# Kernel optimization log

Measured on AMD Instinct MI355X. Metric: run time of the kernel, lower is better.

The kernel has to match this reference:

```python
import jax, jax.numpy as jnp
import numpy as np

D_IN = 1024
D_OUT = 1024

def setup_inputs() -> dict:
    key = jax.random.key(0)
    ks = jax.random.split(key, 7)
    s = 1.0 / np.sqrt(D_IN)
    x = jax.random.normal(ks[0], (4, 2048, D_IN), dtype=jnp.float32)
    Wq = jax.random.uniform(ks[1], (D_IN, D_OUT), jnp.float32, -s, s)
    bq = jax.random.uniform(ks[2], (D_OUT,), jnp.float32, -s, s)
    Wk = jax.random.uniform(ks[3], (D_IN, D_OUT), jnp.float32, -s, s)
    bk = jax.random.uniform(ks[4], (D_OUT,), jnp.float32, -s, s)
    Wv = jax.random.uniform(ks[5], (D_IN, D_OUT), jnp.float32, -s, s)
    bv = jax.random.uniform(ks[6], (D_OUT,), jnp.float32, -s, s)
    return {"x": x, "Wq": Wq, "bq": bq, "Wk": Wk, "bk": bk, "Wv": Wv, "bv": bv}

def reference(x, Wq, bq, Wk, bk, Wv, bv):
    # q,k,v: [B, T, d_out]
    q = x @ Wq + bq
    k = x @ Wk + bk
    v = x @ Wv + bv
    T = x.shape[1]
    scale = 1.0 / jnp.sqrt(jnp.asarray(D_OUT, x.dtype))
    qk = jnp.einsum('btd,bsd->bts', q, k) * scale  # [B, T, T]
    causal = jnp.tril(jnp.ones((T, T), dtype=bool))
    qk = jnp.where(causal, qk, -jnp.inf)
    probs = jax.nn.softmax(qk, axis=-1)
    return jnp.einsum('bts,bsd->btd', probs, v)
```

## Files before the change

### kernel.cpp

```cpp
#include <hip/hip_runtime.h>
#include <cstdint>
#include <cmath>

#define D_MODEL 1024
#define SEQ 2048
#define BATCH 4

typedef short bf16x8 __attribute__((ext_vector_type(8)));
typedef float f32x4 __attribute__((ext_vector_type(4)));

__device__ __forceinline__ short f2bf(float f) {
  union { float f; unsigned int u; } v; v.f = f;
  unsigned int r = (v.u + 0x7FFFu + ((v.u >> 16) & 1u)) >> 16;
  return (short)r;
}

__device__ __forceinline__ float bf2f(short h) {
  union { unsigned int u; float f; } v;
  v.u = ((unsigned int)(unsigned short)h) << 16;
  return v.f;
}

__device__ __forceinline__ f32x4 mfma16(bf16x8 a, bf16x8 b, f32x4 c) {
  return __builtin_amdgcn_mfma_f32_16x16x32_bf16(a, b, c, 0, 0, 0);
}

__device__ __forceinline__ void load_lds16(const void* g, void* l) {
  __builtin_amdgcn_global_load_lds(
      (const __attribute__((address_space(1))) unsigned int*)g,
      (__attribute__((address_space(3))) unsigned int*)l, 16, 0, 0);
}

__global__ __launch_bounds__(256) void convert_x(const float* __restrict__ x,
                                                 short* __restrict__ xb) {
  int i = blockIdx.x * 256 + threadIdx.x;
  float4 f = ((const float4*)x)[i];
  short4 h;
  h.x = f2bf(f.x); h.y = f2bf(f.y); h.z = f2bf(f.z); h.w = f2bf(f.w);
  ((short4*)xb)[i] = h;
}

__global__ __launch_bounds__(256) void transpose_w(const float* __restrict__ Wq,
                                                   const float* __restrict__ Wk,
                                                   const float* __restrict__ Wv,
                                                   short* __restrict__ wt) {
  const int mat = blockIdx.z;
  const float* __restrict__ W = (mat == 0) ? Wq : (mat == 1) ? Wk : Wv;
  short* __restrict__ o = wt + (size_t)mat * (D_MODEL * D_MODEL);
  __shared__ float tile[32][33];
  const int k0 = blockIdx.x * 32, n0 = blockIdx.y * 32;
  const int lx = threadIdx.x & 31, ly = threadIdx.x >> 5;
#pragma unroll
  for (int i = 0; i < 4; ++i) {
    int r = ly + i * 8;
    tile[r][lx] = W[(size_t)(k0 + r) * D_MODEL + n0 + lx];
  }
  __syncthreads();
#pragma unroll
  for (int i = 0; i < 4; ++i) {
    int r = ly + i * 8;
    o[(size_t)(n0 + r) * D_MODEL + k0 + lx] = f2bf(tile[lx][r]);
  }
}

__global__ __launch_bounds__(512, 4) void qkv_gemm(
    const short* __restrict__ xb, const short* __restrict__ wt,
    const float* __restrict__ bq, const float* __restrict__ bk,
    const float* __restrict__ bv, short* __restrict__ qo,
    short* __restrict__ ko, short* __restrict__ vo) {
  const int m0 = blockIdx.x * 256;
  const int n0 = blockIdx.y * 128;
  const int mat = blockIdx.z;
  const short* __restrict__ w = wt + (size_t)mat * (D_MODEL * D_MODEL);
  const float* __restrict__ bias = (mat == 0) ? bq : (mat == 1) ? bk : bv;

  __shared__ short a_lds[2][256 * 32];
  __shared__ short b_lds[2][128 * 32];

  const int tid = threadIdx.x;
  const int wid = tid >> 6;
  const int lane = tid & 63;
  const int quad = lane >> 4;
  const int l16 = lane & 15;
  const int wm = (wid >> 1) * 64;
  const int wn = (wid & 1) * 64;
  const int key = (l16 >> 1) & 3;

  f32x4 acc[4][4] = {};

  auto stage = [&](int k0, int buf) {
#pragma unroll
    for (int h = 0; h < 2; ++h) {
      const int c = tid + h * 512;
      load_lds16(xb + (size_t)(m0 + (c >> 2)) * D_MODEL + k0 +
                     (((c & 3) ^ ((c >> 3) & 3)) << 3),
                 (char*)&a_lds[buf][c * 8]);
    }
    load_lds16(w + (size_t)(n0 + (tid >> 2)) * D_MODEL + k0 +
                   (((tid & 3) ^ ((tid >> 3) & 3)) << 3),
               (char*)&b_lds[buf][tid * 8]);
  };

  stage(0, 0);
  for (int k0 = 0; k0 < D_MODEL; k0 += 32) {
    const int buf = (k0 >> 5) & 1;
    __syncthreads();
    if (k0 + 32 < D_MODEL) stage(k0 + 32, buf ^ 1);
    const short* al = a_lds[buf];
    const short* bl = b_lds[buf];
    bf16x8 af[4], bfr[4];
#pragma unroll
    for (int i = 0; i < 4; ++i)
      af[i] = *(const bf16x8*)(al + (wm + i * 16 + l16) * 32 +
                               ((quad ^ key) << 3));
#pragma unroll
    for (int j = 0; j < 4; ++j)
      bfr[j] = *(const bf16x8*)(bl + (wn + j * 16 + l16) * 32 +
                                ((quad ^ key) << 3));
#pragma unroll
    for (int i = 0; i < 4; ++i)
#pragma unroll
      for (int j = 0; j < 4; ++j)
        acc[i][j] = mfma16(af[i], bfr[j], acc[i][j]);
  }
#pragma unroll
  for (int i = 0; i < 4; ++i) {
#pragma unroll
    for (int j = 0; j < 4; ++j) {
#pragma unroll
      for (int r = 0; r < 4; ++r) {
        const int mrow = m0 + wm + i * 16 + quad * 4 + r;
        const int ncol = n0 + wn + j * 16 + l16;
        const float val = acc[i][j][r] + bias[ncol];
        const short h = f2bf(val);
        if (mat == 2) {
          const int bb = mrow >> 11;
          const int t = mrow & 2047;
          vo[((size_t)bb * D_MODEL + ncol) * SEQ + t] = h;
        } else if (mat == 0) {
          qo[(size_t)mrow * D_MODEL + ncol] = h;
        } else {
          ko[(size_t)mrow * D_MODEL + ncol] = h;
        }
      }
    }
  }
}

__global__ __launch_bounds__(256) void sgemm(const short* __restrict__ qb,
                                             const short* __restrict__ kb,
                                             short* __restrict__ S) {
  if (blockIdx.y > blockIdx.x) return;
  const int m0 = blockIdx.x * 128;
  const int n0 = blockIdx.y * 128;
  const int b = blockIdx.z;
  const short* __restrict__ qp = qb + (size_t)b * SEQ * D_MODEL;
  const short* __restrict__ kp = kb + (size_t)b * SEQ * D_MODEL;

  __shared__ short a_lds[2][128 * 64];
  __shared__ short b_lds[2][128 * 64];

  const int tid = threadIdx.x;
  const int wid = tid >> 6;
  const int lane = tid & 63;
  const int quad = lane >> 4;
  const int l16 = lane & 15;
  const int mw = (wid >> 1) * 64;
  const int nw = (wid & 1) * 64;
  const int sw = l16 & 7;
  const int r_local = wid * 8 + (lane >> 3);
  const int c_sw = ((lane & 7) ^ (lane >> 3)) * 8;

  f32x4 acc[4][4] = {};

  auto stage = [&](int k0, int buf) {
#pragma unroll
    for (int it = 0; it < 4; ++it) {
      load_lds16(qp + (size_t)(m0 + it * 32 + r_local) * D_MODEL + k0 + c_sw,
                 (char*)a_lds[buf] + it * 4096 + wid * 1024);
      load_lds16(kp + (size_t)(n0 + it * 32 + r_local) * D_MODEL + k0 + c_sw,
                 (char*)b_lds[buf] + it * 4096 + wid * 1024);
    }
  };

  stage(0, 0);
  for (int k0 = 0; k0 < D_MODEL; k0 += 64) {
    const int buf = (k0 >> 6) & 1;
    __syncthreads();
    if (k0 + 64 < D_MODEL) stage(k0 + 64, buf ^ 1);
    const short* al = a_lds[buf];
    const short* bl = b_lds[buf];
#pragma unroll
    for (int kt = 0; kt < 2; ++kt) {
      bf16x8 af[4], bfr[4];
#pragma unroll
      for (int i = 0; i < 4; ++i)
        af[i] = *(const bf16x8*)(al + (mw + i * 16 + l16) * 64 +
                                 ((kt * 4 + quad) ^ sw) * 8);
#pragma unroll
      for (int i = 0; i < 4; ++i)
        bfr[i] = *(const bf16x8*)(bl + (nw + i * 16 + l16) * 64 +
                                  ((kt * 4 + quad) ^ sw) * 8);
#pragma unroll
      for (int i = 0; i < 4; ++i)
#pragma unroll
        for (int j = 0; j < 4; ++j)
          acc[i][j] = mfma16(af[i], bfr[j], acc[i][j]);
    }
  }
#pragma unroll
  for (int i = 0; i < 4; ++i) {
#pragma unroll
    for (int j = 0; j < 4; ++j) {
#pragma unroll
      for (int r = 0; r < 4; ++r) {
        const int mrow = m0 + mw + i * 16 + quad * 4 + r;
        const int ncol = n0 + nw + j * 16 + l16;
        S[((size_t)b * SEQ + mrow) * SEQ + ncol] = f2bf(acc[i][j][r] * 0.03125f);
      }
    }
  }
}

__global__ __launch_bounds__(256) void softmax_rows(const short* __restrict__ S,
                                                    short* __restrict__ P) {
  const int row = blockIdx.x;
  const int t = row & (SEQ - 1);
  const int tid = threadIdx.x;
  const short* __restrict__ srow = S + (size_t)row * SEQ;
  short* __restrict__ prow = P + (size_t)row * SEQ;

  __shared__ float red[4];

  float v[8];
#pragma unroll
  for (int i = 0; i < 8; ++i) {
    const int c = tid + i * 256;
    v[i] = (c <= t) ? bf2f(srow[c]) : -1e30f;
  }
  float m = v[0];
#pragma unroll
  for (int i = 1; i < 8; ++i) m = fmaxf(m, v[i]);
#pragma unroll
  for (int o = 32; o; o >>= 1) m = fmaxf(m, __shfl_xor(m, o));
  if ((tid & 63) == 0) red[tid >> 6] = m;
  __syncthreads();
  m = fmaxf(fmaxf(red[0], red[1]), fmaxf(red[2], red[3]));

  float e[8];
  float s = 0.f;
#pragma unroll
  for (int i = 0; i < 8; ++i) {
    e[i] = __expf(v[i] - m);
    s += e[i];
  }
#pragma unroll
  for (int o = 32; o; o >>= 1) s += __shfl_xor(s, o);
  __syncthreads();
  if ((tid & 63) == 0) red[tid >> 6] = s;
  __syncthreads();
  s = red[0] + red[1] + red[2] + red[3];
  const float rinv = 1.0f / s;
  const int nwr = (t >> 8) + 1;
#pragma unroll
  for (int i = 0; i < 8; ++i)
    if (i < nwr) prow[tid + i * 256] = f2bf(e[i] * rinv);
}

__global__ __launch_bounds__(256) void pvgemm(const short* __restrict__ P,
                                              const short* __restrict__ vtb,
                                              float* __restrict__ out) {
  const int n0 = blockIdx.x * 128;
  const int b = blockIdx.y;
  const int m0 = (15 - blockIdx.z) * 128;
  const short* __restrict__ pp = P + (size_t)b * SEQ * SEQ;
  const short* __restrict__ vp = vtb + (size_t)b * D_MODEL * SEQ;
  const int kmax = m0 + 128;

  __shared__ short a_lds[2][128 * 64];
  __shared__ short b_lds[2][128 * 64];

  const int tid = threadIdx.x;
  const int wid = tid >> 6;
  const int lane = tid & 63;
  const int quad = lane >> 4;
  const int l16 = lane & 15;
  const int mw = (wid >> 1) * 64;
  const int nw = (wid & 1) * 64;
  const int sw = l16 & 7;
  const int r_local = wid * 8 + (lane >> 3);
  const int c_sw = ((lane & 7) ^ (lane >> 3)) * 8;

  f32x4 acc[4][4] = {};

  auto stage = [&](int k0, int buf) {
#pragma unroll
    for (int it = 0; it < 4; ++it) {
      load_lds16(pp + (size_t)(m0 + it * 32 + r_local) * SEQ + k0 + c_sw,
                 (char*)a_lds[buf] + it * 4096 + wid * 1024);
      load_lds16(vp + (size_t)(n0 + it * 32 + r_local) * SEQ + k0 + c_sw,
                 (char*)b_lds[buf] + it * 4096 + wid * 1024);
    }
  };

  stage(0, 0);
  for (int k0 = 0; k0 < kmax; k0 += 64) {
    const int buf = (k0 >> 6) & 1;
    __syncthreads();
    if (k0 + 64 < kmax) stage(k0 + 64, buf ^ 1);
    const short* al = a_lds[buf];
    const short* bl = b_lds[buf];
#pragma unroll
    for (int kt = 0; kt < 2; ++kt) {
      bf16x8 af[4], bfr[4];
#pragma unroll
      for (int i = 0; i < 4; ++i)
        af[i] = *(const bf16x8*)(al + (mw + i * 16 + l16) * 64 +
                                 ((kt * 4 + quad) ^ sw) * 8);
#pragma unroll
      for (int i = 0; i < 4; ++i)
        bfr[i] = *(const bf16x8*)(bl + (nw + i * 16 + l16) * 64 +
                                  ((kt * 4 + quad) ^ sw) * 8);
#pragma unroll
      for (int i = 0; i < 4; ++i)
#pragma unroll
        for (int j = 0; j < 4; ++j)
          acc[i][j] = mfma16(af[i], bfr[j], acc[i][j]);
    }
  }
#pragma unroll
  for (int i = 0; i < 4; ++i) {
#pragma unroll
    for (int j = 0; j < 4; ++j) {
#pragma unroll
      for (int r = 0; r < 4; ++r) {
        const int mrow = m0 + mw + i * 16 + quad * 4 + r;
        const int ncol = n0 + nw + j * 16 + l16;
        out[((size_t)b * SEQ + mrow) * D_MODEL + ncol] = acc[i][j][r];
      }
    }
  }
}

extern "C" void kernel_launch(void* const* d_in, const int* in_sizes, int n_in,
                              void* d_out, int out_size, void* d_ws, size_t ws_size,
                              hipStream_t stream) {
  (void)in_sizes; (void)n_in; (void)out_size; (void)ws_size;
  const float* x  = (const float*)d_in[0];
  const float* Wq = (const float*)d_in[1];
  const float* bq = (const float*)d_in[2];
  const float* Wk = (const float*)d_in[3];
  const float* bk = (const float*)d_in[4];
  const float* Wv = (const float*)d_in[5];
  const float* bv = (const float*)d_in[6];
  float* out = (float*)d_out;

  char* ws = (char*)d_ws;
  short* xb = (short*)(ws);
  short* wt = (short*)(ws + 16777216);
  short* qo = (short*)(ws + 23068672);
  short* ko = (short*)(ws + 39845888);
  short* vo = (short*)(ws + 56623104);
  short* S  = (short*)(ws + 73400320);
  short* P  = (short*)(ws);

  convert_x<<<dim3(8192), dim3(256), 0, stream>>>(x, xb);
  transpose_w<<<dim3(32, 32, 3), dim3(256), 0, stream>>>(Wq, Wk, Wv, wt);
  qkv_gemm<<<dim3(32, 8, 3), dim3(512), 0, stream>>>(xb, wt, bq, bk, bv, qo, ko, vo);
  sgemm<<<dim3(16, 16, BATCH), dim3(256), 0, stream>>>(qo, ko, S);
  softmax_rows<<<dim3(BATCH * SEQ), dim3(256), 0, stream>>>(S, P);
  pvgemm<<<dim3(8, BATCH, 16), dim3(256), 0, stream>>>(P, vo, out);
}
```

Before: 263.3 us.

## Triple-buffer LDS with register-prefetched fragments across GEMMs; compact causal sgemm grid

```diff
diff --git a/kernel.cpp b/kernel.cpp
--- a/kernel.cpp
+++ b/kernel.cpp
@@ -63,27 +63,28 @@
   }
 }
 
-__global__ __launch_bounds__(512, 4) void qkv_gemm(
+
+__global__ __launch_bounds__(256) void qkv_gemm(
     const short* __restrict__ xb, const short* __restrict__ wt,
     const float* __restrict__ bq, const float* __restrict__ bk,
     const float* __restrict__ bv, short* __restrict__ qo,
     short* __restrict__ ko, short* __restrict__ vo) {
-  const int m0 = blockIdx.x * 256;
+  const int m0 = blockIdx.x * 128;
   const int n0 = blockIdx.y * 128;
   const int mat = blockIdx.z;
   const short* __restrict__ w = wt + (size_t)mat * (D_MODEL * D_MODEL);
   const float* __restrict__ bias = (mat == 0) ? bq : (mat == 1) ? bk : bv;
 
-  __shared__ short a_lds[2][256 * 32];
-  __shared__ short b_lds[2][128 * 32];
+  __shared__ short a_lds[3][128 * 32];
+  __shared__ short b_lds[3][128 * 32];
 
   const int tid = threadIdx.x;
   const int wid = tid >> 6;
   const int lane = tid & 63;
   const int quad = lane >> 4;
   const int l16 = lane & 15;
-  const int wm = (wid >> 1) * 64;
-  const int wn = (wid & 1) * 64;
+  const int mw = (wid >> 1) * 64;
+  const int nw = (wid & 1) * 64;
   const int key = (l16 >> 1) & 3;
 
   f32x4 acc[4][4] = {};
@@ -91,37 +92,50 @@
   auto stage = [&](int k0, int buf) {
 #pragma unroll
     for (int h = 0; h < 2; ++h) {
-      const int c = tid + h * 512;
-      load_lds16(xb + (size_t)(m0 + (c >> 2)) * D_MODEL + k0 +
-                     (((c & 3) ^ ((c >> 3) & 3)) << 3),
+      const int c = tid + h * 256;
+      const int gc = ((c & 3) ^ ((c >> 3) & 3)) << 3;
+      load_lds16(xb + (size_t)(m0 + (c >> 2)) * D_MODEL + k0 + gc,
                  (char*)&a_lds[buf][c * 8]);
-    }
-    load_lds16(w + (size_t)(n0 + (tid >> 2)) * D_MODEL + k0 +
-                   (((tid & 3) ^ ((tid >> 3) & 3)) << 3),
-               (char*)&b_lds[buf][tid * 8]);
-  };
-
-  stage(0, 0);
-  for (int k0 = 0; k0 < D_MODEL; k0 += 32) {
-    const int buf = (k0 >> 5) & 1;
-    __syncthreads();
-    if (k0 + 32 < D_MODEL) stage(k0 + 32, buf ^ 1);
+      load_lds16(w + (size_t)(n0 + (c >> 2)) * D_MODEL + k0 + gc,
+                 (char*)&b_lds[buf][c * 8]);
+    }
+  };
+  auto read_frags = [&](int buf, bf16x8* af, bf16x8* bfr) {
     const short* al = a_lds[buf];
     const short* bl = b_lds[buf];
-    bf16x8 af[4], bfr[4];
-#pragma unroll
-    for (int i = 0; i < 4; ++i)
-      af[i] = *(const bf16x8*)(al + (wm + i * 16 + l16) * 32 +
-                               ((quad ^ key) << 3));
+#pragma unroll
+    for (int i = 0; i < 4; ++i)
+      af[i] = *(const bf16x8*)(al + (mw + i * 16 + l16) * 32 + ((quad ^ key) << 3));
 #pragma unroll
     for (int j = 0; j < 4; ++j)
-      bfr[j] = *(const bf16x8*)(bl + (wn + j * 16 + l16) * 32 +
-                                ((quad ^ key) << 3));
+      bfr[j] = *(const bf16x8*)(bl + (nw + j * 16 + l16) * 32 + ((quad ^ key) << 3));
+  };
+  auto domfma = [&](bf16x8* af, bf16x8* bfr) {
 #pragma unroll
     for (int i = 0; i < 4; ++i)
 #pragma unroll
       for (int j = 0; j < 4; ++j)
         acc[i][j] = mfma16(af[i], bfr[j], acc[i][j]);
+  };
+
+  const int NIT = D_MODEL / 32;
+  stage(0, 0);
+  stage(32, 1);
+  __syncthreads();
+  bf16x8 af0[4], bf0[4], af1[4], bf1[4];
+  read_frags(0, af0, bf0);
+  int b0 = 0, b1 = 1, b2 = 2;
+  for (int k = 0; k < NIT; k += 2) {
+    const int kk = k * 32;
+    if (k + 2 < NIT) stage(kk + 64, b2);
+    read_frags(b1, af1, bf1);
+    domfma(af0, bf0);
+    __syncthreads();
+    if (k + 3 < NIT) stage(kk + 96, b0);
+    if (k + 2 < NIT) read_frags(b2, af0, bf0);
+    domfma(af1, bf1);
+    __syncthreads();
+    const int t0 = b0; b0 = b2; b2 = b1; b1 = t0;
   }
 #pragma unroll
   for (int i = 0; i < 4; ++i) {
@@ -129,8 +143,8 @@
     for (int j = 0; j < 4; ++j) {
 #pragma unroll
       for (int r = 0; r < 4; ++r) {
-        const int mrow = m0 + wm + i * 16 + quad * 4 + r;
-        const int ncol = n0 + wn + j * 16 + l16;
+        const int mrow = m0 + mw + i * 16 + quad * 4 + r;
+        const int ncol = n0 + nw + j * 16 + l16;
         const float val = acc[i][j][r] + bias[ncol];
         const short h = f2bf(val);
         if (mat == 2) {
@@ -150,15 +164,18 @@
 __global__ __launch_bounds__(256) void sgemm(const short* __restrict__ qb,
                                              const short* __restrict__ kb,
                                              short* __restrict__ S) {
-  if (blockIdx.y > blockIdx.x) return;
-  const int m0 = blockIdx.x * 128;
-  const int n0 = blockIdx.y * 128;
-  const int b = blockIdx.z;
+  const int t = blockIdx.x;
+  int r = (int)((sqrtf(8.0f * t + 1.0f) - 1.0f) * 0.5f);
+  while ((r + 1) * (r + 2) / 2 <= t) ++r;
+  while (r * (r + 1) / 2 > t) --r;
+  const int m0 = r * 128;
+  const int n0 = (t - r * (r + 1) / 2) * 128;
+  const int b = blockIdx.y;
   const short* __restrict__ qp = qb + (size_t)b * SEQ * D_MODEL;
   const short* __restrict__ kp = kb + (size_t)b * SEQ * D_MODEL;
 
-  __shared__ short a_lds[2][128 * 64];
-  __shared__ short b_lds[2][128 * 64];
+  __shared__ short a_lds[3][128 * 32];
+  __shared__ short b_lds[3][128 * 32];
 
   const int tid = threadIdx.x;
   const int wid = tid >> 6;
@@ -167,56 +184,67 @@
   const int l16 = lane & 15;
   const int mw = (wid >> 1) * 64;
   const int nw = (wid & 1) * 64;
-  const int sw = l16 & 7;
-  const int r_local = wid * 8 + (lane >> 3);
-  const int c_sw = ((lane & 7) ^ (lane >> 3)) * 8;
+  const int key = (l16 >> 1) & 3;
 
   f32x4 acc[4][4] = {};
 
   auto stage = [&](int k0, int buf) {
 #pragma unroll
-    for (int it = 0; it < 4; ++it) {
-      load_lds16(qp + (size_t)(m0 + it * 32 + r_local) * D_MODEL + k0 + c_sw,
-                 (char*)a_lds[buf] + it * 4096 + wid * 1024);
-      load_lds16(kp + (size_t)(n0 + it * 32 + r_local) * D_MODEL + k0 + c_sw,
-                 (char*)b_lds[buf] + it * 4096 + wid * 1024);
-    }
-  };
-
-  stage(0, 0);
-  for (int k0 = 0; k0 < D_MODEL; k0 += 64) {
-    const int buf = (k0 >> 6) & 1;
-    __syncthreads();
-    if (k0 + 64 < D_MODEL) stage(k0 + 64, buf ^ 1);
+    for (int h = 0; h < 2; ++h) {
+      const int c = tid + h * 256;
+      const int gc = ((c & 3) ^ ((c >> 3) & 3)) << 3;
+      load_lds16(qp + (size_t)(m0 + (c >> 2)) * D_MODEL + k0 + gc,
+                 (char*)&a_lds[buf][c * 8]);
+      load_lds16(kp + (size_t)(n0 + (c >> 2)) * D_MODEL + k0 + gc,
+                 (char*)&b_lds[buf][c * 8]);
+    }
+  };
+  auto read_frags = [&](int buf, bf16x8* af, bf16x8* bfr) {
     const short* al = a_lds[buf];
     const short* bl = b_lds[buf];
 #pragma unroll
-    for (int kt = 0; kt < 2; ++kt) {
-      bf16x8 af[4], bfr[4];
-#pragma unroll
-      for (int i = 0; i < 4; ++i)
-        af[i] = *(const bf16x8*)(al + (mw + i * 16 + l16) * 64 +
-                                 ((kt * 4 + quad) ^ sw) * 8);
-#pragma unroll
-      for (int i = 0; i < 4; ++i)
-        bfr[i] = *(const bf16x8*)(bl + (nw + i * 16 + l16) * 64 +
-                                  ((kt * 4 + quad) ^ sw) * 8);
-#pragma unroll
-      for (int i = 0; i < 4; ++i)
-#pragma unroll
-        for (int j = 0; j < 4; ++j)
-          acc[i][j] = mfma16(af[i], bfr[j], acc[i][j]);
-    }
+    for (int i = 0; i < 4; ++i)
+      af[i] = *(const bf16x8*)(al + (mw + i * 16 + l16) * 32 + ((quad ^ key) << 3));
+#pragma unroll
+    for (int j = 0; j < 4; ++j)
+      bfr[j] = *(const bf16x8*)(bl + (nw + j * 16 + l16) * 32 + ((quad ^ key) << 3));
+  };
+  auto domfma = [&](bf16x8* af, bf16x8* bfr) {
+#pragma unroll
+    for (int i = 0; i < 4; ++i)
+#pragma unroll
+      for (int j = 0; j < 4; ++j)
+        acc[i][j] = mfma16(af[i], bfr[j], acc[i][j]);
+  };
+
+  const int NIT = D_MODEL / 32;
+  stage(0, 0);
+  stage(32, 1);
+  __syncthreads();
+  bf16x8 af0[4], bf0[4], af1[4], bf1[4];
+  read_frags(0, af0, bf0);
+  int b0 = 0, b1 = 1, b2 = 2;
+  for (int k = 0; k < NIT; k += 2) {
+    const int kk = k * 32;
+    if (k + 2 < NIT) stage(kk + 64, b2);
+    read_frags(b1, af1, bf1);
+    domfma(af0, bf0);
+    __syncthreads();
+    if (k + 3 < NIT) stage(kk + 96, b0);
+    if (k + 2 < NIT) read_frags(b2, af0, bf0);
+    domfma(af1, bf1);
+    __syncthreads();
+    const int t0 = b0; b0 = b2; b2 = b1; b1 = t0;
   }
 #pragma unroll
   for (int i = 0; i < 4; ++i) {
 #pragma unroll
     for (int j = 0; j < 4; ++j) {
 #pragma unroll
-      for (int r = 0; r < 4; ++r) {
-        const int mrow = m0 + mw + i * 16 + quad * 4 + r;
+      for (int rr = 0; rr < 4; ++rr) {
+        const int mrow = m0 + mw + i * 16 + quad * 4 + rr;
         const int ncol = n0 + nw + j * 16 + l16;
-        S[((size_t)b * SEQ + mrow) * SEQ + ncol] = f2bf(acc[i][j][r] * 0.03125f);
+        S[((size_t)b * SEQ + mrow) * SEQ + ncol] = f2bf(acc[i][j][rr] * 0.03125f);
       }
     }
   }
@@ -275,10 +303,9 @@
   const int m0 = (15 - blockIdx.z) * 128;
   const short* __restrict__ pp = P + (size_t)b * SEQ * SEQ;
   const short* __restrict__ vp = vtb + (size_t)b * D_MODEL * SEQ;
-  const int kmax = m0 + 128;
-
-  __shared__ short a_lds[2][128 * 64];
-  __shared__ short b_lds[2][128 * 64];
+
+  __shared__ short a_lds[3][128 * 32];
+  __shared__ short b_lds[3][128 * 32];
 
   const int tid = threadIdx.x;
   const int wid = tid >> 6;
@@ -287,46 +314,57 @@
   const int l16 = lane & 15;
   const int mw = (wid >> 1) * 64;
   const int nw = (wid & 1) * 64;
-  const int sw = l16 & 7;
-  const int r_local = wid * 8 + (lane >> 3);
-  const int c_sw = ((lane & 7) ^ (lane >> 3)) * 8;
+  const int key = (l16 >> 1) & 3;
 
   f32x4 acc[4][4] = {};
 
   auto stage = [&](int k0, int buf) {
 #pragma unroll
-    for (int it = 0; it < 4; ++it) {
-      load_lds16(pp + (size_t)(m0 + it * 32 + r_local) * SEQ + k0 + c_sw,
-                 (char*)a_lds[buf] + it * 4096 + wid * 1024);
-      load_lds16(vp + (size_t)(n0 + it * 32 + r_local) * SEQ + k0 + c_sw,
-                 (char*)b_lds[buf] + it * 4096 + wid * 1024);
-    }
-  };
-
-  stage(0, 0);
-  for (int k0 = 0; k0 < kmax; k0 += 64) {
-    const int buf = (k0 >> 6) & 1;
-    __syncthreads();
-    if (k0 + 64 < kmax) stage(k0 + 64, buf ^ 1);
+    for (int h = 0; h < 2; ++h) {
+      const int c = tid + h * 256;
+      const int gc = ((c & 3) ^ ((c >> 3) & 3)) << 3;
+      load_lds16(pp + (size_t)(m0 + (c >> 2)) * SEQ + k0 + gc,
+                 (char*)&a_lds[buf][c * 8]);
+      load_lds16(vp + (size_t)(n0 + (c >> 2)) * SEQ + k0 + gc,
+                 (char*)&b_lds[buf][c * 8]);
+    }
+  };
+  auto read_frags = [&](int buf, bf16x8* af, bf16x8* bfr) {
     const short* al = a_lds[buf];
     const short* bl = b_lds[buf];
 #pragma unroll
-    for (int kt = 0; kt < 2; ++kt) {
-      bf16x8 af[4], bfr[4];
-#pragma unroll
-      for (int i = 0; i < 4; ++i)
-        af[i] = *(const bf16x8*)(al + (mw + i * 16 + l16) * 64 +
-                                 ((kt * 4 + quad) ^ sw) * 8);
-#pragma unroll
-      for (int i = 0; i < 4; ++i)
-        bfr[i] = *(const bf16x8*)(bl + (nw + i * 16 + l16) * 64 +
-                                  ((kt * 4 + quad) ^ sw) * 8);
-#pragma unroll
-      for (int i = 0; i < 4; ++i)
-#pragma unroll
-        for (int j = 0; j < 4; ++j)
-          acc[i][j] = mfma16(af[i], bfr[j], acc[i][j]);
-    }
+    for (int i = 0; i < 4; ++i)
+      af[i] = *(const bf16x8*)(al + (mw + i * 16 + l16) * 32 + ((quad ^ key) << 3));
+#pragma unroll
+    for (int j = 0; j < 4; ++j)
+      bfr[j] = *(const bf16x8*)(bl + (nw + j * 16 + l16) * 32 + ((quad ^ key) << 3));
+  };
+  auto domfma = [&](bf16x8* af, bf16x8* bfr) {
+#pragma unroll
+    for (int i = 0; i < 4; ++i)
+#pragma unroll
+      for (int j = 0; j < 4; ++j)
+        acc[i][j] = mfma16(af[i], bfr[j], acc[i][j]);
+  };
+
+  const int NIT = (m0 + 128) / 32;
+  stage(0, 0);
+  stage(32, 1);
+  __syncthreads();
+  bf16x8 af0[4], bf0[4], af1[4], bf1[4];
+  read_frags(0, af0, bf0);
+  int b0 = 0, b1 = 1, b2 = 2;
+  for (int k = 0; k < NIT; k += 2) {
+    const int kk = k * 32;
+    if (k + 2 < NIT) stage(kk + 64, b2);
+    read_frags(b1, af1, bf1);
+    domfma(af0, bf0);
+    __syncthreads();
+    if (k + 3 < NIT) stage(kk + 96, b0);
+    if (k + 2 < NIT) read_frags(b2, af0, bf0);
+    domfma(af1, bf1);
+    __syncthreads();
+    const int t0 = b0; b0 = b2; b2 = b1; b1 = t0;
   }
 #pragma unroll
   for (int i = 0; i < 4; ++i) {
@@ -366,8 +404,8 @@
 
   convert_x<<<dim3(8192), dim3(256), 0, stream>>>(x, xb);
   transpose_w<<<dim3(32, 32, 3), dim3(256), 0, stream>>>(Wq, Wk, Wv, wt);
-  qkv_gemm<<<dim3(32, 8, 3), dim3(512), 0, stream>>>(xb, wt, bq, bk, bv, qo, ko, vo);
-  sgemm<<<dim3(16, 16, BATCH), dim3(256), 0, stream>>>(qo, ko, S);
+  qkv_gemm<<<dim3(64, 8, 3), dim3(256), 0, stream>>>(xb, wt, bq, bk, bv, qo, ko, vo);
+  sgemm<<<dim3(136, BATCH), dim3(256), 0, stream>>>(qo, ko, S);
   softmax_rows<<<dim3(BATCH * SEQ), dim3(256), 0, stream>>>(S, P);
   pvgemm<<<dim3(8, BATCH, 16), dim3(256), 0, stream>>>(P, vo, out);
 }
```

After: 278.8 us. 5.9% more time.
